# Optimization experiments

Hardware: AMD Instinct MI355X
Metric: run time of the kernel (lower is better)

## Reference

```python
import jax, jax.numpy as jnp
import numpy as np

# ---- config (from init_kwargs) ----
BASE_SIZE = 16
RATIOS = np.array([0.5, 1.0, 2.0])
N_LAYERS = 3
SCALES = 2.0 ** np.arange(N_LAYERS)
STRIDE = 16
PRE_NMS_TOPN = 2000
POST_NMS_TOPN = 300
MIN_THRESHOLD = 16.0
NMS_THRESH = 0.7
IMG_W = 1024
IMG_H = 1024
B, H, W = 16, 64, 64
A = len(RATIOS) * len(SCALES)  # 9


def _whctrs(a):
    w = a[2] - a[0] + 1.0
    h = a[3] - a[1] + 1.0
    return w, h, a[0] + 0.5 * (w - 1.0), a[1] + 0.5 * (h - 1.0)


def _mkanchors(ws, hs, cx, cy):
    return np.stack([cx - 0.5 * (ws - 1.0), cy - 0.5 * (hs - 1.0),
                     cx + 0.5 * (ws - 1.0), cy + 0.5 * (hs - 1.0)], axis=1)


def _generate_anchors():
    base = np.array([0.0, 0.0, BASE_SIZE - 1.0, BASE_SIZE - 1.0])
    w, h, cx, cy = _whctrs(base)
    size = w * h
    ws = np.round(np.sqrt(size / RATIOS))
    hs = np.round(ws * RATIOS)
    ratio_anchors = _mkanchors(ws, hs, np.full_like(ws, cx), np.full_like(ws, cy))
    out = []
    for ra in ratio_anchors:
        rw, rh, rcx, rcy = _whctrs(ra)
        out.append(_mkanchors(rw * SCALES, rh * SCALES,
                              np.full_like(SCALES, rcx), np.full_like(SCALES, rcy)))
    return np.concatenate(out, axis=0)  # (A, 4)


def _all_anchors(height, width):
    anchors = _generate_anchors()  # (A, 4)
    sx = np.arange(width) * STRIDE
    sy = np.arange(height) * STRIDE
    sx, sy = np.meshgrid(sx, sy)  # (H, W) row-major over y -> matches permute(0,2,3,1)
    shifts = np.stack([sx.ravel(), sy.ravel(), sx.ravel(), sy.ravel()], axis=1)  # (K, 4)
    return (anchors[None, :, :] + shifts[:, None, :]).reshape(-1, 4).astype(np.float32)  # (K*A, 4)


def _decode(deltas, anchors):
    # bbox_reg_to_coord: standard bbox_transform_inv
    aw = anchors[:, 2] - anchors[:, 0] + 1.0
    ah = anchors[:, 3] - anchors[:, 1] + 1.0
    acx = anchors[:, 0] + 0.5 * aw
    acy = anchors[:, 1] + 0.5 * ah
    cx = deltas[..., 0] * aw + acx
    cy = deltas[..., 1] * ah + acy
    pw = jnp.exp(deltas[..., 2]) * aw
    ph = jnp.exp(deltas[..., 3]) * ah
    return jnp.stack([cx - 0.5 * pw, cy - 0.5 * ph,
                      cx + 0.5 * pw, cy + 0.5 * ph], axis=-1)


def _nms_single(boxes, scores):
    # boxes: (N, 4) sorted by descending score
    N = boxes.shape[0]
    x1, y1, x2, y2 = boxes[:, 0], boxes[:, 1], boxes[:, 2], boxes[:, 3]
    areas = (x2 - x1 + 1.0) * (y2 - y1 + 1.0)
    iw = jnp.maximum(0.0, jnp.minimum(x2[:, None], x2[None, :]) - jnp.maximum(x1[:, None], x1[None, :]) + 1.0)
    ih = jnp.maximum(0.0, jnp.minimum(y2[:, None], y2[None, :]) - jnp.maximum(y1[:, None], y1[None, :]) + 1.0)
    inter = iw * ih
    iou = inter / (areas[:, None] + areas[None, :] - inter)  # (N, N)
    idx = jnp.arange(N)

    def body(sup, i):  # greedy sequential NMS
        keep_i = ~sup[i]
        sup = sup | (keep_i & (iou[i] > NMS_THRESH) & (idx > i))
        return sup, keep_i

    _, keep = jax.lax.scan(body, jnp.zeros(N, dtype=bool), idx)
    # kept boxes first, preserving score order; fixed-size output padded with zeros
    prio = jnp.where(keep, idx, idx + N)
    order = jnp.argsort(prio)[:POST_NMS_TOPN]
    valid = keep[order]
    out_boxes = jnp.where(valid[:, None], boxes[order], 0.0)
    out_scores = jnp.where(valid, scores[order], 0.0)
    return out_boxes, out_scores


def reference(labels_pred, bbox_reg):
    b, _, h, w = labels_pred.shape
    anchors = jnp.asarray(_all_anchors(h, w))  # (K*A, 4)
    scores = labels_pred.transpose(0, 2, 3, 1).reshape(b, -1, 2)[..., 1]  # (B, K*A)
    deltas = bbox_reg.transpose(0, 2, 3, 1).reshape(b, -1, 4)  # (B, K*A, 4)
    boxes = _decode(deltas, anchors)
    boxes = jnp.stack([
        jnp.clip(boxes[..., 0], 0.0, IMG_W - 1.0),
        jnp.clip(boxes[..., 1], 0.0, IMG_H - 1.0),
        jnp.clip(boxes[..., 2], 0.0, IMG_W - 1.0),
        jnp.clip(boxes[..., 3], 0.0, IMG_H - 1.0)], axis=-1)
    keep = ((boxes[..., 2] - boxes[..., 0] + 1.0 >= MIN_THRESHOLD)
            & (boxes[..., 3] - boxes[..., 1] + 1.0 >= MIN_THRESHOLD))
    masked = jnp.where(keep, scores, -jnp.inf)
    top_scores, top_idx = jax.lax.top_k(masked, PRE_NMS_TOPN)  # (B, pre)
    top_boxes = jnp.take_along_axis(boxes, top_idx[..., None], axis=1)  # (B, pre, 4)
    return jax.vmap(_nms_single)(top_boxes, top_scores)


def setup_inputs() -> dict:
    key = jax.random.key(0)
    k1, k2 = jax.random.split(key)
    labels_pred = jax.random.normal(k1, (B, 2 * A, H, W), dtype=jnp.float32)
    bbox_reg = jax.random.normal(k2, (B, 4 * A, H, W), dtype=jnp.float32) * 0.2
    return {"labels_pred": labels_pred, "bbox_reg": bbox_reg}
```

## Files before the change

kernel.cpp:

```cpp
#include <hip/hip_runtime.h>
#include <stdint.h>

#pragma clang fp contract(off)

typedef unsigned long long ull;

#define NB 16
#define NA 9
#define HW 4096
#define NANCH (NA*HW)
#define TOTAL (NB*NANCH)
#define TOPN 2000
#define PADN 2048
#define SELPAD 3072
#define OUTN 300
#define HBITS 13
#define HBINS (1 << HBITS)
#define MNMS 768
#define MSTRIPS (MNMS/64)
#define MPITCH 16
#define GD2 16

#define MIDC 0x1.666667p-1

__constant__ float c_ax1[9] = {-3.5f,-15.f,-38.f,  0.f, -8.f,-24.f,  2.5f, -3.f,-14.f};
__constant__ float c_ay1[9] = { 2.f,  -4.f,-16.f,  0.f, -8.f,-24.f, -3.f,-14.f,-36.f};
__constant__ float c_ax2[9] = {18.5f, 30.f, 53.f, 15.f, 23.f, 39.f, 12.5f, 18.f, 29.f};
__constant__ float c_ay2[9] = {13.f,  19.f, 31.f, 15.f, 23.f, 39.f, 18.f,  29.f, 51.f};

__device__ __forceinline__ void decode_box(int a, int x, int y,
    float d0, float d1, float d2, float d3,
    float& x1, float& y1, float& x2, float& y2) {
  float ax1 = c_ax1[a] + 16.f * (float)x;
  float ay1 = c_ay1[a] + 16.f * (float)y;
  float ax2 = c_ax2[a] + 16.f * (float)x;
  float ay2 = c_ay2[a] + 16.f * (float)y;
  float aw  = ax2 - ax1 + 1.f;
  float ah  = ay2 - ay1 + 1.f;
  float acx = ax1 + 0.5f * aw;
  float acy = ay1 + 0.5f * ah;
  float cx = d0 * aw + acx;
  float cy = d1 * ah + acy;
  float pw = expf(d2) * aw;
  float ph = expf(d3) * ah;
  x1 = cx - 0.5f * pw;
  y1 = cy - 0.5f * ph;
  x2 = cx + 0.5f * pw;
  y2 = cy + 0.5f * ph;
  x1 = fminf(fmaxf(x1, 0.f), 1023.f);
  y1 = fminf(fmaxf(y1, 0.f), 1023.f);
  x2 = fminf(fmaxf(x2, 0.f), 1023.f);
  y2 = fminf(fmaxf(y2, 0.f), 1023.f);
}

__device__ __forceinline__ uint32_t f2ord(float f) {
  uint32_t u = __float_as_uint(f);
  return (u & 0x80000000u) ? ~u : (u | 0x80000000u);
}
__device__ __forceinline__ float ord2f(uint32_t u) {
  return (u & 0x80000000u) ? __uint_as_float(u ^ 0x80000000u) : __uint_as_float(~u);
}

__global__ void k_score(const float* __restrict__ labels, const float* __restrict__ bbox,
                        uint32_t* __restrict__ keys) {
  int t4 = blockIdx.x * 256 + threadIdx.x;
  int p4 = t4 & 1023;
  int pos = p4 << 2;
  int ba = t4 >> 10;
  int a = ba % 9, b = ba / 9;
  float4 sc  = ((const float4*)(labels + ((b * 18 + 2 * a + 1) << 12)))[p4];
  const float* dpb = bbox + ((b * 36 + 4 * a) << 12);
  float4 d0v = ((const float4*)(dpb        ))[p4];
  float4 d1v = ((const float4*)(dpb +  4096))[p4];
  float4 d2v = ((const float4*)(dpb +  8192))[p4];
  float4 d3v = ((const float4*)(dpb + 12288))[p4];
  int y = pos >> 6, x0 = pos & 63;
  float scA[4] = { sc.x,  sc.y,  sc.z,  sc.w  };
  float d0A[4] = { d0v.x, d0v.y, d0v.z, d0v.w };
  float d1A[4] = { d1v.x, d1v.y, d1v.z, d1v.w };
  float d2A[4] = { d2v.x, d2v.y, d2v.z, d2v.w };
  float d3A[4] = { d3v.x, d3v.y, d3v.z, d3v.w };
  uint32_t kout[4];
#pragma unroll
  for (int k = 0; k < 4; ++k) {
    float x1, y1, x2, y2;
    decode_box(a, x0 + k, y, d0A[k], d1A[k], d2A[k], d3A[k], x1, y1, x2, y2);
    bool keep = (x2 - x1 + 1.f >= 16.f) && (y2 - y1 + 1.f >= 16.f);
    kout[k] = f2ord(keep ? scA[k] : -INFINITY);
  }
  ((uint4*)(keys + b * NANCH + (a << 12) + pos))[0] =
      make_uint4(kout[0], kout[1], kout[2], kout[3]);
}

__global__ __launch_bounds__(1024) void k_batch(const uint32_t* __restrict__ keys,
                                                ull* __restrict__ selKeys,
                                                uint32_t* __restrict__ counters) {
  int b = blockIdx.x, tid = threadIdx.x;
  int wave = tid >> 6, lane = tid & 63;
  __shared__ uint32_t hist[HBINS];
  __shared__ uint32_t wtot[16];
  __shared__ uint32_t sh_T, sh_cnt;
  const uint32_t* kb = keys + b * NANCH;
  const uint4* kb4 = (const uint4*)kb;
#pragma unroll
  for (int k = 0; k < HBINS / 1024; ++k) hist[k * 1024 + tid] = 0u;
  if (tid == 0) { sh_T = 0u; sh_cnt = 0u; }
  __syncthreads();
  for (int i4 = tid; i4 < NANCH / 4; i4 += 1024) {
    uint4 v = kb4[i4];
    if (v.x & 0x80000000u) atomicAdd(&hist[v.x >> (32 - HBITS)], 1u);
    if (v.y & 0x80000000u) atomicAdd(&hist[v.y >> (32 - HBITS)], 1u);
    if (v.z & 0x80000000u) atomicAdd(&hist[v.z >> (32 - HBITS)], 1u);
    if (v.w & 0x80000000u) atomicAdd(&hist[v.w >> (32 - HBITS)], 1u);
  }
  __syncthreads();
  uint32_t c[8], suf[8];
#pragma unroll
  for (int k = 0; k < 8; ++k) c[k] = hist[tid * 8 + k];
  suf[7] = c[7];
#pragma unroll
  for (int k = 6; k >= 0; --k) suf[k] = c[k] + suf[k + 1];
  uint32_t total = suf[0];
  uint32_t wsuf = total;
#pragma unroll
  for (int off = 1; off < 64; off <<= 1) {
    uint32_t v = __shfl_down(wsuf, off);
    if (lane + off < 64) wsuf += v;
  }
  if (lane == 0) wtot[wave] = wsuf;
  __syncthreads();
  uint32_t wab = 0;
  for (int w = wave + 1; w < 16; ++w) wab += wtot[w];
  uint32_t ssum = wsuf + wab;
  uint32_t above_t = ssum - total;
  if (above_t < TOPN && ssum >= TOPN) {
    uint32_t T = (uint32_t)(tid * 8);
#pragma unroll
    for (int k = 7; k >= 0; --k) {
      uint32_t ab = above_t + ((k < 7) ? suf[k + 1] : 0u);
      if (ab < TOPN && ab + c[k] >= TOPN) T = (uint32_t)(tid * 8 + k);
    }
    sh_T = T;
  }
  __syncthreads();
  uint32_t T = sh_T;
  for (int i4 = tid; i4 < NANCH / 4; i4 += 1024) {
    uint4 v = kb4[i4];
    uint32_t vv[4] = { v.x, v.y, v.z, v.w };
#pragma unroll
    for (int cc = 0; cc < 4; ++cc) {
      uint32_t u = vv[cc];
      if ((u >> (32 - HBITS)) >= T) {
        uint32_t slot = atomicAdd(&sh_cnt, 1u);
        if (slot < SELPAD) {
          int i = i4 * 4 + cc;
          uint32_t canon = (uint32_t)((i & 4095) * 9 + (i >> 12));
          selKeys[b * SELPAD + slot] = (((ull)(~u)) << 32) | canon;
        }
      }
    }
  }
  __syncthreads();
  if (tid == 0) counters[b] = (sh_cnt < SELPAD) ? sh_cnt : SELPAD;
}

__global__ __launch_bounds__(256) void k_rank(const ull* __restrict__ selKeys,
                        const uint32_t* __restrict__ counters, const float* __restrict__ bbox,
                        float4* __restrict__ boxes, float* __restrict__ areas,
                        float* __restrict__ selScore) {
  int b = blockIdx.y;
  int i = blockIdx.x * 256 + threadIdx.x;
  int tid = threadIdx.x;
  uint32_t n = counters[b];
  const ull* sk = selKeys + b * SELPAD;
  ull ki = (i < (int)n) ? sk[i] : ~0ull;
  int rank = 0;
  __shared__ ull chunk[256];
  for (uint32_t base = 0; base < n; base += 256) {
    uint32_t j = base + (uint32_t)tid;
    chunk[tid] = (j < n) ? sk[j] : ~0ull;
    __syncthreads();
    int lim = (int)(n - base < 256u ? n - base : 256u);
    for (int t2 = 0; t2 < lim; ++t2) rank += (chunk[t2] < ki) ? 1 : 0;
    __syncthreads();
  }
  if (i < (int)n && rank < TOPN) {
    uint32_t idx = (uint32_t)ki;
    selScore[b * TOPN + rank] = ord2f(~((uint32_t)(ki >> 32)));
    int pos = (int)idx / 9, a = (int)idx - 9 * pos;
    int y = pos >> 6, x = pos & 63;
    const float* dp = bbox + ((b * 36 + 4 * a) << 12) + pos;
    float d0 = dp[0], d1 = dp[4096], d2 = dp[8192], d3 = dp[12288];
    float x1, y1, x2, y2;
    decode_box(a, x, y, d0, d1, d2, d3, x1, y1, x2, y2);
    boxes[b * PADN + rank] = make_float4(x1, y1, x2, y2);
    areas[b * PADN + rank] = (x2 - x1 + 1.f) * (y2 - y1 + 1.f);
  }
}

__global__ __launch_bounds__(256) void k_mask(const float4* __restrict__ boxes,
                                              const float* __restrict__ areas,
                                              ull* __restrict__ gmask) {
  int rb = blockIdx.x, b = blockIdx.y;
  int tid = threadIdx.x, wv = tid >> 6, lane = tid & 63;
  int rbase = rb * 32;
  int smin = rbase >> 6;
  __shared__ float4 sRow[32];
  __shared__ float  sAr[32];
  if (tid < 32) {
    sRow[tid] = boxes[b * PADN + rbase + tid];
    sAr[tid]  = areas[b * PADN + rbase + tid];
  }
  float4 bj[MSTRIPS];
  float  ja[MSTRIPS];
#pragma unroll
  for (int s = 0; s < MSTRIPS; ++s) {
    if (s >= smin) {
      bj[s] = boxes[b * PADN + (s << 6) + lane];
      ja[s] = areas[b * PADN + (s << 6) + lane];
    }
  }
  __syncthreads();
  const double MD = MIDC;
  for (int r = wv; r < 32; r += 4) {
    int i = rbase + r;
    float4 bi = sRow[r];
    float  ia = sAr[r];
#pragma unroll
    for (int s = 0; s < MSTRIPS; ++s) {
      if (s < smin) continue;
      int j = (s << 6) + lane;
      float iw = fminf(bi.z, bj[s].z) - fmaxf(bi.x, bj[s].x) + 1.f; iw = fmaxf(iw, 0.f);
      float ih = fminf(bi.w, bj[s].w) - fmaxf(bi.y, bj[s].y) + 1.f; ih = fmaxf(ih, 0.f);
      float inter = iw * ih;
      float uu = (ia + ja[s]) - inter;
      bool sup = (j > i) && ((double)inter >= MD * (double)uu);
      ull mb = __ballot(sup);
      if (lane == 0) gmask[((size_t)b * MNMS + i) * MPITCH + s] = mb;
    }
  }
}

__global__ __launch_bounds__(64) void k_scan(const ull* __restrict__ gmask,
                                             const float4* __restrict__ boxes,
                                             const float* __restrict__ areas,
                                             const float* __restrict__ selScore,
                                             float* __restrict__ out) {
  int b = blockIdx.x, lane = threadIdx.x;
  const ull* mb = gmask + (size_t)b * MNMS * MPITCH;
  int l16 = lane & 15;
  __shared__ int kidx[OUTN];
  __shared__ int sh_cnt;
  const double MD = MIDC;
  ull supw = 0ull;
  int cnt = 0;
  ull pf[GD2];
#pragma unroll
  for (int ph = 0; ph < GD2; ++ph) pf[ph] = mb[ph * MPITCH + l16];
  for (int base = 0; base < MNMS && cnt < OUTN; base += GD2) {
#pragma unroll
    for (int ph = 0; ph < GD2; ++ph) {
      int i = base + ph;
      ull bal = __ballot(((supw >> (i & 63)) & 1ull) != 0ull);
      if (!((bal >> (i >> 6)) & 1ull)) {
        ull mm = (l16 >= (i >> 6) && l16 < MSTRIPS) ? pf[ph] : 0ull;
        supw |= mm;
        if (lane == 0 && cnt < OUTN) kidx[cnt] = i;
        cnt++;
      }
      int nx = i + GD2; if (nx > MNMS - 1) nx = MNMS - 1;
      pf[ph] = mb[nx * MPITCH + l16];
    }
  }
  for (int i = MNMS; i < TOPN && cnt < OUTN; ++i) {
    float4 bi = boxes[b * PADN + i];
    float ia = areas[b * PADN + i];
    bool sup = false;
    for (int cb = 0; cb < cnt; cb += 64) {
      int k = cb + lane;
      if (k < cnt) {
        int kj = kidx[k];
        float4 bk = boxes[b * PADN + kj];
        float ka = areas[b * PADN + kj];
        float iw = fminf(bi.z, bk.z) - fmaxf(bi.x, bk.x) + 1.f; iw = fmaxf(iw, 0.f);
        float ih = fminf(bi.w, bk.w) - fmaxf(bi.y, bk.y) + 1.f; ih = fmaxf(ih, 0.f);
        float inter = iw * ih;
        float uu = (ia + ka) - inter;
        sup = sup || ((double)inter >= MD * (double)uu);
      }
    }
    if (!__any(sup)) {
      if (lane == 0) kidx[cnt] = i;
      cnt++;
    }
  }
  if (lane == 0) sh_cnt = (cnt < OUTN) ? cnt : OUTN;
  __syncthreads();
  int c = sh_cnt;
  float4* ob = (float4*)out;
  for (int s2 = lane; s2 < OUTN; s2 += 64) {
    float4 bx = make_float4(0.f, 0.f, 0.f, 0.f);
    float sc = 0.f;
    if (s2 < c) {
      int i = kidx[s2];
      bx = boxes[b * PADN + i];
      sc = selScore[b * TOPN + i];
    }
    ob[b * OUTN + s2] = bx;
    out[NB * OUTN * 4 + b * OUTN + s2] = sc;
  }
}

extern "C" void kernel_launch(void* const* d_in, const int* in_sizes, int n_in,
                              void* d_out, int out_size, void* d_ws, size_t ws_size,
                              hipStream_t stream) {
  const float* labels = (const float*)d_in[0];
  const float* bbox   = (const float*)d_in[1];
  char* ws = (char*)d_ws;
  uint32_t* keys    = (uint32_t*)(ws + 0);
  ull* selKeys      = (ull*)(ws + 2359296);
  float* selScore   = (float*)(ws + 2752512);
  float* areas      = (float*)(ws + 2880512);
  float4* boxes     = (float4*)(ws + 3011584);
  uint32_t* counters= (uint32_t*)(ws + 3535872);
  ull* gmask        = (ull*)(ws + 3535936);
  float* out = (float*)d_out;

  hipLaunchKernelGGL(k_score, dim3(TOTAL / 4 / 256), dim3(256), 0, stream, labels, bbox, keys);
  hipLaunchKernelGGL(k_batch, dim3(NB), dim3(1024), 0, stream, keys, selKeys, counters);
  hipLaunchKernelGGL(k_rank,  dim3(SELPAD / 256, NB), dim3(256), 0, stream, selKeys, counters, bbox, boxes, areas, selScore);
  hipLaunchKernelGGL(k_mask,  dim3(MNMS / 32, NB), dim3(256), 0, stream, boxes, areas, gmask);
  hipLaunchKernelGGL(k_scan,  dim3(NB), dim3(64), 0, stream, gmask, boxes, areas, selScore, out);
}
```

Before: 97.86 us.

## Build full NMS suppression bitmask and scan it with double-buffered 32-bit chunks

The bitmask kernel now covers all 2000 candidates instead of the first 768. It launches over row blocks, strip groups and batches, and exits early for blocks entirely below the diagonal. The serial IoU fallback for candidates past 768 is removed. The scan walks 32-bit mask words, tracks the diagonal word in a register so it no longer needs a wave ballot per candidate, and double-buffers mask prefetch across chunks. In exchange the mask computation and workspace grow considerably, and the scan may read more memory when many candidates are needed.

```diff
diff --git a/kernel.cpp b/kernel.cpp
--- a/kernel.cpp
+++ b/kernel.cpp
@@ -16,10 +16,9 @@
 #define OUTN 300
 #define HBITS 13
 #define HBINS (1 << HBITS)
-#define MNMS 768
-#define MSTRIPS (MNMS/64)
-#define MPITCH 16
-#define GD2 16
+#define MROWS 2048
+#define MW 32
+#define SG 8
 
 #define MIDC 0x1.666667p-1
 
@@ -201,24 +200,25 @@
 __global__ __launch_bounds__(256) void k_mask(const float4* __restrict__ boxes,
                                               const float* __restrict__ areas,
                                               ull* __restrict__ gmask) {
-  int rb = blockIdx.x, b = blockIdx.y;
-  int tid = threadIdx.x, wv = tid >> 6, lane = tid & 63;
+  int rb = blockIdx.x, g = blockIdx.y, b = blockIdx.z;
   int rbase = rb * 32;
   int smin = rbase >> 6;
+  int s0 = g * SG;
+  if (s0 + SG - 1 < smin) return;
+  int tid = threadIdx.x, wv = tid >> 6, lane = tid & 63;
   __shared__ float4 sRow[32];
   __shared__ float  sAr[32];
   if (tid < 32) {
     sRow[tid] = boxes[b * PADN + rbase + tid];
     sAr[tid]  = areas[b * PADN + rbase + tid];
   }
-  float4 bj[MSTRIPS];
-  float  ja[MSTRIPS];
-#pragma unroll
-  for (int s = 0; s < MSTRIPS; ++s) {
-    if (s >= smin) {
-      bj[s] = boxes[b * PADN + (s << 6) + lane];
-      ja[s] = areas[b * PADN + (s << 6) + lane];
-    }
+  float4 bj[SG];
+  float  ja[SG];
+#pragma unroll
+  for (int s = 0; s < SG; ++s) {
+    int j = ((s0 + s) << 6) + lane;
+    bj[s] = boxes[b * PADN + j];
+    ja[s] = areas[b * PADN + j];
   }
   __syncthreads();
   const double MD = MIDC;
@@ -227,73 +227,75 @@
     float4 bi = sRow[r];
     float  ia = sAr[r];
 #pragma unroll
-    for (int s = 0; s < MSTRIPS; ++s) {
-      if (s < smin) continue;
-      int j = (s << 6) + lane;
+    for (int s = 0; s < SG; ++s) {
+      int j = ((s0 + s) << 6) + lane;
       float iw = fminf(bi.z, bj[s].z) - fmaxf(bi.x, bj[s].x) + 1.f; iw = fmaxf(iw, 0.f);
       float ih = fminf(bi.w, bj[s].w) - fmaxf(bi.y, bj[s].y) + 1.f; ih = fmaxf(ih, 0.f);
       float inter = iw * ih;
       float uu = (ia + ja[s]) - inter;
-      bool sup = (j > i) && ((double)inter >= MD * (double)uu);
+      bool sup = (j < TOPN) && (j > i) && ((double)inter >= MD * (double)uu);
       ull mb = __ballot(sup);
-      if (lane == 0) gmask[((size_t)b * MNMS + i) * MPITCH + s] = mb;
+      if (lane == 0 && i < TOPN) gmask[((size_t)b * MROWS + i) * MW + (s0 + s)] = mb;
     }
   }
 }
 
 __global__ __launch_bounds__(64) void k_scan(const ull* __restrict__ gmask,
                                              const float4* __restrict__ boxes,
-                                             const float* __restrict__ areas,
                                              const float* __restrict__ selScore,
                                              float* __restrict__ out) {
   int b = blockIdx.x, lane = threadIdx.x;
-  const ull* mb = gmask + (size_t)b * MNMS * MPITCH;
-  int l16 = lane & 15;
+  const uint32_t* mrows = (const uint32_t*)(gmask + (size_t)b * MROWS * MW);
   __shared__ int kidx[OUTN];
   __shared__ int sh_cnt;
-  const double MD = MIDC;
-  ull supw = 0ull;
+  uint32_t supw = 0u;
   int cnt = 0;
-  ull pf[GD2];
-#pragma unroll
-  for (int ph = 0; ph < GD2; ++ph) pf[ph] = mb[ph * MPITCH + l16];
-  for (int base = 0; base < MNMS && cnt < OUTN; base += GD2) {
-#pragma unroll
-    for (int ph = 0; ph < GD2; ++ph) {
-      int i = base + ph;
-      ull bal = __ballot(((supw >> (i & 63)) & 1ull) != 0ull);
-      if (!((bal >> (i >> 6)) & 1ull)) {
-        ull mm = (l16 >= (i >> 6) && l16 < MSTRIPS) ? pf[ph] : 0ull;
-        supw |= mm;
-        if (lane == 0 && cnt < OUTN) kidx[cnt] = i;
-        cnt++;
-      }
-      int nx = i + GD2; if (nx > MNMS - 1) nx = MNMS - 1;
-      pf[ph] = mb[nx * MPITCH + l16];
-    }
-  }
-  for (int i = MNMS; i < TOPN && cnt < OUTN; ++i) {
-    float4 bi = boxes[b * PADN + i];
-    float ia = areas[b * PADN + i];
-    bool sup = false;
-    for (int cb = 0; cb < cnt; cb += 64) {
-      int k = cb + lane;
-      if (k < cnt) {
-        int kj = kidx[k];
-        float4 bk = boxes[b * PADN + kj];
-        float ka = areas[b * PADN + kj];
-        float iw = fminf(bi.z, bk.z) - fmaxf(bi.x, bk.x) + 1.f; iw = fmaxf(iw, 0.f);
-        float ih = fminf(bi.w, bk.w) - fmaxf(bi.y, bk.y) + 1.f; ih = fmaxf(ih, 0.f);
-        float inter = iw * ih;
-        float uu = (ia + ka) - inter;
-        sup = sup || ((double)inter >= MD * (double)uu);
-      }
-    }
-    if (!__any(sup)) {
-      if (lane == 0) kidx[cnt] = i;
-      cnt++;
-    }
-  }
+  uint32_t mA[32], dA[32], mB[32], dB[32];
+#pragma unroll
+  for (int ph = 0; ph < 32; ++ph) {
+    mA[ph] = mrows[ph * 64 + lane];
+    dA[ph] = mrows[ph * 64 + 0];
+  }
+
+#define PREFETCH(MARR, DARR, CN)                                             \
+  {                                                                          \
+    int cn_ = (CN) > 62 ? 62 : (CN);                                         \
+    _Pragma("unroll")                                                        \
+    for (int ph = 0; ph < 32; ++ph) {                                        \
+      int r = cn_ * 32 + ph;                                                 \
+      MARR[ph] = mrows[r * 64 + lane];                                       \
+      DARR[ph] = mrows[r * 64 + cn_];                                        \
+    }                                                                        \
+  }
+
+#define CHUNK(CC, MARR, DARR)                                                \
+  {                                                                          \
+    uint32_t sw = __shfl(supw, (CC));                                        \
+    _Pragma("unroll")                                                        \
+    for (int ph = 0; ph < 32; ++ph) {                                        \
+      int i = (CC) * 32 + ph;                                                \
+      uint32_t t = (sw >> ph) & 1u;                                          \
+      if (i >= TOPN) t = 1u;                                                 \
+      uint32_t keepm = t - 1u;                        \
+      uint32_t mm = (lane >= (uint32_t)((i >> 6) << 1)) ? MARR[ph] : 0u;     \
+      supw |= mm & keepm;                                                    \
+      sw   |= DARR[ph] & keepm;                                              \
+      if (lane == 0 && t == 0u && cnt < OUTN) kidx[cnt] = i;                 \
+      cnt += (int)(t ^ 1u);                                                  \
+    }                                                                        \
+  }
+
+  for (int cc = 0; cc < 63; cc += 2) {
+    PREFETCH(mB, dB, cc + 1);
+    CHUNK(cc, mA, dA);
+    if (cnt >= OUTN) break;
+    PREFETCH(mA, dA, cc + 2);
+    CHUNK(cc + 1, mB, dB);
+    if (cnt >= OUTN) break;
+  }
+#undef CHUNK
+#undef PREFETCH
+
   if (lane == 0) sh_cnt = (cnt < OUTN) ? cnt : OUTN;
   __syncthreads();
   int c = sh_cnt;
@@ -329,6 +331,6 @@
   hipLaunchKernelGGL(k_score, dim3(TOTAL / 4 / 256), dim3(256), 0, stream, labels, bbox, keys);
   hipLaunchKernelGGL(k_batch, dim3(NB), dim3(1024), 0, stream, keys, selKeys, counters);
   hipLaunchKernelGGL(k_rank,  dim3(SELPAD / 256, NB), dim3(256), 0, stream, selKeys, counters, bbox, boxes, areas, selScore);
-  hipLaunchKernelGGL(k_mask,  dim3(MNMS / 32, NB), dim3(256), 0, stream, boxes, areas, gmask);
-  hipLaunchKernelGGL(k_scan,  dim3(NB), dim3(64), 0, stream, gmask, boxes, areas, selScore, out);
-}
+  hipLaunchKernelGGL(k_mask,  dim3(63, 4, NB), dim3(256), 0, stream, boxes, areas, gmask);
+  hipLaunchKernelGGL(k_scan,  dim3(NB), dim3(64), 0, stream, gmask, boxes, selScore, out);
+}
```

Result: slower. 111.8 us (+14.3%).
